# Kernel tuning notes

Measured on AMD Instinct MI355X. Metric: run time of the kernel, lower is better.

The kernel has to match this reference:

```python
import jax, jax.numpy as jnp
import numpy as np

N, E, DIN, H, EIN, EH, STEPS = 10000, 100000, 64, 64, 16, 128, 3


def setup_inputs() -> dict:
    key = jax.random.key(0)
    ks = jax.random.split(key, 8)
    n_feat = jax.random.normal(ks[0], (N, DIN), jnp.float32)
    e_feat = jax.random.normal(ks[1], (E, EIN), jnp.float32)
    src = jax.random.randint(ks[2], (E,), 0, N, jnp.int32)
    dst = jax.random.randint(ks[3], (E,), 0, N, jnp.int32)
    W0 = jax.random.normal(ks[4], (DIN, H), jnp.float32) / np.sqrt(DIN)
    b0 = jnp.zeros((H,), jnp.float32)
    We1 = jax.random.normal(ks[5], (EIN, EH), jnp.float32) / np.sqrt(EIN)
    be1 = jnp.zeros((EH,), jnp.float32)
    # small scale so per-edge HxH weight matrices keep activations stable
    We2 = jax.random.normal(ks[6], (EH, H * H), jnp.float32) * 0.02
    be2 = jnp.zeros((H * H,), jnp.float32)
    conv_bias = jnp.zeros((H,), jnp.float32)
    gamma = jnp.ones((H,), jnp.float32)
    beta = jnp.zeros((H,), jnp.float32)
    return {"n_feat": n_feat, "e_feat": e_feat, "src": src, "dst": dst,
            "W0": W0, "b0": b0, "We1": We1, "be1": be1, "We2": We2,
            "be2": be2, "conv_bias": conv_bias, "gamma": gamma, "beta": beta}


def reference(n_feat, e_feat, src, dst, W0, b0, We1, be1, We2, be2, conv_bias, gamma, beta):
    n = n_feat.shape[0]
    h = W0.shape[1]
    out = jax.nn.relu(n_feat @ W0 + b0)  # [N,H]
    # edge network (eval mode: dropout = identity); e_feat is fixed so the
    # per-edge weight matrices are identical each step -> compute once.
    w_edge = (jax.nn.relu(e_feat @ We1 + be1) @ We2 + be2).reshape(-1, h, h)  # [E,H,H]
    for _ in range(STEPS):
        msg = jnp.einsum('ei,eio->eo', out[src], w_edge)  # gather + per-edge matmul
        agg = jax.ops.segment_sum(msg, dst, num_segments=n)  # scatter-sum to dst
        out = jax.nn.relu(agg + conv_bias)
    # BatchNorm1d over nodes (training-mode batch statistics)
    mean = jnp.mean(out, axis=0)
    var = jnp.var(out, axis=0)
    return (out - mean) * jax.lax.rsqrt(var + 1e-5) * gamma + beta
```

## Files before the change

### kernel.cpp

```cpp
#include <hip/hip_runtime.h>
#include <stdint.h>

#define DIN   64
#define HDIM  64
#define EIN   16
#define EHID  128
#define HH    4096
#define TC    8256
#define STEPS 3

typedef short bf16x8 __attribute__((ext_vector_type(8)));
typedef float f32x4  __attribute__((ext_vector_type(4)));

__device__ __forceinline__ unsigned short f32_to_bf16(float f) {
    union { float f; uint32_t u; } v; v.f = f;
    uint32_t r = v.u + 0x7fffu + ((v.u >> 16) & 1u);
    return (unsigned short)(r >> 16);
}
__device__ __forceinline__ float bfu_to_f(unsigned short u) {
    union { uint32_t u; float f; } v; v.u = (uint32_t)u << 16; return v.f;
}

__global__ void k_pro(const float* __restrict__ nf, const float* __restrict__ W0,
                      const float* __restrict__ b0, float* __restrict__ outb,
                      unsigned short* __restrict__ outbf,
                      const float* __restrict__ ef, const float* __restrict__ We1,
                      const float* __restrict__ be1, unsigned short* __restrict__ h,
                      const float* __restrict__ We2, const float* __restrict__ be2,
                      unsigned short* __restrict__ BmatT,
                      const int* __restrict__ src, const int* __restrict__ dst,
                      int* __restrict__ cntS, int* __restrict__ cntD,
                      int n_nodes, int n_edges, int nbN, int nbE, int nbB) {
    __shared__ float smem[DIN * HDIM];
    int b = blockIdx.x, tid = threadIdx.x;
    if (b < nbN) {
        for (int i = tid; i < DIN * HDIM; i += 256) smem[i] = W0[i];
        __syncthreads();
        int node = b * 4 + (tid >> 6);
        int o = tid & 63;
        if (node >= n_nodes) return;
        float xr = nf[node * DIN + o];
        float acc = b0[o];
#pragma unroll 8
        for (int i = 0; i < DIN; ++i)
            acc += __shfl(xr, i, 64) * smem[i * HDIM + o];
        float v = fmaxf(acc, 0.f);
        outb[node * HDIM + o] = v;
        outbf[node * HDIM + o] = f32_to_bf16(v);
    } else if (b < nbN + nbE) {
        float* w1s = smem;
        float* xs  = smem + EIN * EHID;
        int e0 = (b - nbN) * 16;
#pragma unroll
        for (int i = tid; i < EIN * EHID; i += 256) w1s[i] = We1[i];
        xs[tid] = ef[(size_t)e0 * EIN + tid];
        __syncthreads();
        int g = tid >> 4, c0 = (tid & 15) * 8;
        int edge = e0 + g;
        if (edge >= n_edges) return;
        float acc[8];
#pragma unroll
        for (int j = 0; j < 8; ++j) acc[j] = be1[c0 + j];
#pragma unroll
        for (int i = 0; i < EIN; ++i) {
            float xi = xs[g * EIN + i];
#pragma unroll
            for (int j = 0; j < 8; ++j) acc[j] += xi * w1s[i * EHID + c0 + j];
        }
        uint32_t p0 = f32_to_bf16(fmaxf(acc[0], 0.f)) | ((uint32_t)f32_to_bf16(fmaxf(acc[1], 0.f)) << 16);
        uint32_t p1 = f32_to_bf16(fmaxf(acc[2], 0.f)) | ((uint32_t)f32_to_bf16(fmaxf(acc[3], 0.f)) << 16);
        uint32_t p2 = f32_to_bf16(fmaxf(acc[4], 0.f)) | ((uint32_t)f32_to_bf16(fmaxf(acc[5], 0.f)) << 16);
        uint32_t p3 = f32_to_bf16(fmaxf(acc[6], 0.f)) | ((uint32_t)f32_to_bf16(fmaxf(acc[7], 0.f)) << 16);
        uint4 pk = {p0, p1, p2, p3};
        *(uint4*)(h + (size_t)edge * EHID + c0) = pk;
    } else if (b < nbN + nbE + nbB) {
        int t = (b - nbN - nbE) * 256 + tid;
        if (t >= TC * 64) return;
        int c = t >> 6, i = t & 63;
        int g = c & 63;
        int m = (c & ~63) + 4 * (g & 15) + (g >> 4);
        float v;
        if (m < 8192) {
            int k = ((m >> 11) << 5) | (m & 31);
            int o = (m >> 5) & 63;
            v = We2[k * HH + i * 64 + o];
        } else {
            v = be2[i * 64 + (m - 8192)];
        }
        BmatT[t] = f32_to_bf16(v);
    } else {
        int e = (b - nbN - nbE - nbB) * 256 + tid;
        if (e >= n_edges) return;
        atomicAdd(&cntS[src[e]], 1);
        atomicAdd(&cntD[dst[e]], 1);
    }
}

__global__ void k_T(const unsigned short* __restrict__ outbf, const unsigned short* __restrict__ BmatT,
                    unsigned short* __restrict__ T, int n0, int n1) {
    int wave = threadIdx.x >> 6, lane = threadIdx.x & 63;
    int r = lane & 15, q = lane >> 4;
    int eb = n0 + blockIdx.y * 128;
    int cb = blockIdx.x * 256 + wave * 64;
    bf16x8 bfr[4][2];
#pragma unroll
    for (int nt = 0; nt < 4; ++nt) {
        int c = cb + nt * 16 + r;
        if (c >= TC) c = 0;
        size_t cofs = (size_t)c * 64;
        bfr[nt][0] = *(const bf16x8*)(BmatT + cofs + q * 8);
        bfr[nt][1] = *(const bf16x8*)(BmatT + cofs + 32 + q * 8);
    }
    bool cok = (cb < TC);
#pragma unroll
    for (int mt = 0; mt < 8; ++mt) {
        int e = eb + mt * 16 + r;
        if (e >= n1) e = n1 - 1;
        bf16x8 afr0 = *(const bf16x8*)(outbf + (size_t)e * 64 + q * 8);
        bf16x8 afr1 = *(const bf16x8*)(outbf + (size_t)e * 64 + 32 + q * 8);
        f32x4 acc[4] = {};
#pragma unroll
        for (int nt = 0; nt < 4; ++nt) {
            acc[nt] = __builtin_amdgcn_mfma_f32_16x16x32_bf16(afr0, bfr[nt][0], acc[nt], 0, 0, 0);
            acc[nt] = __builtin_amdgcn_mfma_f32_16x16x32_bf16(afr1, bfr[nt][1], acc[nt], 0, 0, 0);
        }
        if (!cok) continue;
#pragma unroll
        for (int rg = 0; rg < 4; ++rg) {
            int n = eb + mt * 16 + q * 4 + rg;
            if (n >= n1) continue;
            ushort4 pk;
            pk.x = f32_to_bf16(acc[0][rg]);
            pk.y = f32_to_bf16(acc[1][rg]);
            pk.z = f32_to_bf16(acc[2][rg]);
            pk.w = f32_to_bf16(acc[3][rg]);
            *(ushort4*)(T + (size_t)(n - n0) * TC + cb + 4 * r) = pk;
        }
    }
}

__global__ void k_msg(const unsigned short* __restrict__ h, const unsigned short* __restrict__ T,
                      const int* __restrict__ offS, const int* __restrict__ permS,
                      float* __restrict__ msg, int n0, int n1) {
    int wave = threadIdx.x >> 6, lane = threadIdx.x & 63;
    int n = n0 + blockIdx.x * 4 + wave;
    if (n >= n1) return;
    int beg = offS[n], end = offS[n + 1];
    if (beg == end) return;
    int r = lane & 15, q = lane >> 4;
    const unsigned short* Tb = T + (size_t)(n - n0) * TC;
    float bias[4];
#pragma unroll
    for (int nt = 0; nt < 4; ++nt)
        bias[nt] = bfu_to_f(Tb[8192 + nt * 16 + r]);
    for (int j0 = beg; j0 < end; j0 += 16) {
        int jc = j0 + r; if (jc >= end) jc = end - 1;
        int e = permS[jc];
        const unsigned short* he = h + (size_t)e * EHID;
        f32x4 acc[4] = {};
#pragma unroll
        for (int s = 0; s < 4; ++s) {
            bf16x8 afr = *(const bf16x8*)(he + s * 32 + q * 8);
#pragma unroll
            for (int nt = 0; nt < 4; ++nt) {
                bf16x8 bfr = *(const bf16x8*)(Tb + s * 2048 + (nt * 16 + r) * 32 + q * 8);
                acc[nt] = __builtin_amdgcn_mfma_f32_16x16x32_bf16(afr, bfr, acc[nt], 0, 0, 0);
            }
        }
#pragma unroll
        for (int rg = 0; rg < 4; ++rg) {
            int jr = j0 + q * 4 + rg;
            if (jr >= end) continue;
            int er = permS[jr];
#pragma unroll
            for (int nt = 0; nt < 4; ++nt)
                msg[(size_t)er * 64 + nt * 16 + r] = acc[nt][rg] + bias[nt];
        }
    }
}

__global__ void k_scan(const int* __restrict__ cntS, const int* __restrict__ cntD,
                       int* __restrict__ offS, int* __restrict__ offD,
                       int* __restrict__ curS, int* __restrict__ curD, int n, int total) {
    const int* cnt = blockIdx.x ? cntD : cntS;
    int* off = blockIdx.x ? offD : offS;
    int* cur = blockIdx.x ? curD : curS;
    __shared__ int part[256];
    int tid = threadIdx.x;
    int chunk = (n + 255) / 256;
    int c0 = tid * chunk, c1 = c0 + chunk; if (c1 > n) c1 = n; if (c0 > n) c0 = n;
    int s = 0;
    for (int i = c0; i < c1; ++i) s += cnt[i];
    part[tid] = s;
    __syncthreads();
    for (int st = 1; st < 256; st <<= 1) {
        int v = (tid >= st) ? part[tid - st] : 0;
        __syncthreads();
        part[tid] += v;
        __syncthreads();
    }
    int run = tid ? part[tid - 1] : 0;
    for (int i = c0; i < c1; ++i) { off[i] = run; cur[i] = run; run += cnt[i]; }
    if (tid == 0) off[n] = total;
}

__global__ void k_perm(const int* __restrict__ src, const int* __restrict__ dst,
                       int* __restrict__ curS, int* __restrict__ curD,
                       int* __restrict__ permS, int* __restrict__ permD, int n_edges) {
    int e = blockIdx.x * 256 + threadIdx.x;
    if (e >= n_edges) return;
    permS[atomicAdd(&curS[src[e]], 1)] = e;
    permD[atomicAdd(&curD[dst[e]], 1)] = e;
}

__global__ void k_agg(const float* __restrict__ msg, const int* __restrict__ offD,
                      const int* __restrict__ permD, const float* __restrict__ cbias,
                      float* __restrict__ outb, unsigned short* __restrict__ outbf, int n_nodes) {
    int wave = threadIdx.x >> 6, lane = threadIdx.x & 63;
    int d = blockIdx.x * 4 + wave;
    if (d >= n_nodes) return;
    float acc = 0.f;
    int end = offD[d + 1];
    for (int j = offD[d]; j < end; ++j)
        acc += msg[(size_t)permD[j] * 64 + lane];
    float v = fmaxf(acc + cbias[lane], 0.f);
    outb[(size_t)d * 64 + lane] = v;
    outbf[(size_t)d * 64 + lane] = f32_to_bf16(v);
}

__global__ void k_bn_stats(const float* __restrict__ out, float* __restrict__ stat, int n_nodes) {
    __shared__ float s1[256], s2[256];
    int tid = threadIdx.x;
    int f = tid & 63, g = tid >> 6;
    float sum = 0.f, ss = 0.f;
    for (int r = blockIdx.x * 4 + g; r < n_nodes; r += 256) {
        float v = out[r * HDIM + f];
        sum += v; ss += v * v;
    }
    s1[tid] = sum; s2[tid] = ss;
    __syncthreads();
    if (tid < 64) {
        float A = s1[tid] + s1[64 + tid] + s1[128 + tid] + s1[192 + tid];
        float B = s2[tid] + s2[64 + tid] + s2[128 + tid] + s2[192 + tid];
        atomicAdd(&stat[tid], A);
        atomicAdd(&stat[64 + tid], B);
    }
}

__global__ void k_bn_apply(const float* __restrict__ out, const float* __restrict__ stat,
                           const float* __restrict__ gamma, const float* __restrict__ beta,
                           float* __restrict__ y, int n, int n_nodes) {
    int t = blockIdx.x * 256 + threadIdx.x;
    if (t >= n) return;
    int f = t & 63;
    float mean = stat[f] / n_nodes;
    float var  = stat[64 + f] / n_nodes - mean * mean;
    float inv  = rsqrtf(var + 1e-5f);
    float scale = gamma[f] * inv;
    float shift = beta[f] - mean * scale;
    y[t] = out[t] * scale + shift;
}

extern "C" void kernel_launch(void* const* d_in, const int* in_sizes, int n_in,
                              void* d_out, int out_size, void* d_ws, size_t ws_size,
                              hipStream_t stream) {
    const float* nf    = (const float*)d_in[0];
    const float* ef    = (const float*)d_in[1];
    const int*   src   = (const int*)d_in[2];
    const int*   dst   = (const int*)d_in[3];
    const float* W0    = (const float*)d_in[4];
    const float* b0    = (const float*)d_in[5];
    const float* We1   = (const float*)d_in[6];
    const float* be1   = (const float*)d_in[7];
    const float* We2   = (const float*)d_in[8];
    const float* be2   = (const float*)d_in[9];
    const float* cbias = (const float*)d_in[10];
    const float* gamma = (const float*)d_in[11];
    const float* beta  = (const float*)d_in[12];
    (void)n_in; (void)out_size;

    int n_nodes = in_sizes[0] / DIN;
    int n_edges = in_sizes[2];

    char* ws = (char*)d_ws;
    size_t off = 0;
    auto carve = [&](size_t bytes) -> void* {
        void* p = ws + off;
        off = (off + bytes + 255) & ~(size_t)255;
        return p;
    };
    unsigned short* h     = (unsigned short*)carve((size_t)n_edges * EHID * 2);
    float*          msg   = (float*)carve((size_t)n_edges * 64 * 4);
    float*          outb  = (float*)carve((size_t)n_nodes * HDIM * 4);
    unsigned short* outbf = (unsigned short*)carve((size_t)n_nodes * HDIM * 2);
    unsigned short* BmatT = (unsigned short*)carve((size_t)TC * 64 * 2);
    int*            offS  = (int*)carve((size_t)(n_nodes + 1) * 4);
    int*            offD  = (int*)carve((size_t)(n_nodes + 1) * 4);
    int*            curS  = (int*)carve((size_t)n_nodes * 4);
    int*            curD  = (int*)carve((size_t)n_nodes * 4);
    int*            permS = (int*)carve((size_t)n_edges * 4);
    int*            permD = (int*)carve((size_t)n_edges * 4);
    float*          stat  = (float*)carve(128 * 4 + (size_t)2 * n_nodes * 4);
    int*            cntS  = (int*)(stat + 128);
    int*            cntD  = cntS + n_nodes;
    unsigned short* T     = (unsigned short*)(ws + off);
    size_t avail = ws_size > off ? ws_size - off : 0;
    long tcap = (long)(avail / ((size_t)TC * 2));
    if (tcap > n_nodes) tcap = n_nodes;
    if (tcap < 64) tcap = 64;
    long half = (((long)n_nodes + 1) / 2 + 63) & ~63L;
    long tchunk = tcap < half ? tcap : half;

    hipMemsetAsync(stat, 0, 128 * 4 + (size_t)2 * n_nodes * 4, stream);

    int nbN = (n_nodes + 3) / 4;
    int nbE = (n_edges + 15) / 16;
    int nbB = (TC * 64 + 255) / 256;
    int nbH = (n_edges + 255) / 256;
    k_pro<<<dim3(nbN + nbE + nbB + nbH), 256, 0, stream>>>(
        nf, W0, b0, outb, outbf, ef, We1, be1, h, We2, be2, BmatT,
        src, dst, cntS, cntD, n_nodes, n_edges, nbN, nbE, nbB);
    k_scan<<<dim3(2), 256, 0, stream>>>(cntS, cntD, offS, offD, curS, curD, n_nodes, n_edges);
    k_perm<<<dim3((n_edges + 255) / 256), 256, 0, stream>>>(src, dst, curS, curD, permS, permD, n_edges);

    for (int step = 0; step < STEPS; ++step) {
        for (long n0 = 0; n0 < n_nodes; n0 += tchunk) {
            long n1 = n0 + tchunk; if (n1 > n_nodes) n1 = n_nodes;
            long cnt = n1 - n0;
            k_T<<<dim3((TC + 255) / 256, (cnt + 127) / 128), 256, 0, stream>>>(
                outbf, BmatT, T, (int)n0, (int)n1);
            k_msg<<<dim3((cnt + 3) / 4), 256, 0, stream>>>(
                h, T, offS, permS, msg, (int)n0, (int)n1);
        }
        k_agg<<<dim3((n_nodes + 3) / 4), 256, 0, stream>>>(msg, offD, permD, cbias, outb, outbf, n_nodes);
    }

    k_bn_stats<<<dim3(64), 256, 0, stream>>>(outb, stat, n_nodes);
    k_bn_apply<<<dim3((n_nodes * HDIM + 255) / 256), 256, 0, stream>>>(
        outb, stat, gamma, beta, (float*)d_out, n_nodes * HDIM, n_nodes);
}
```

Before: 481.3 us.

## Compute edge hidden layer with MFMA and drop forced node-chunk halving

```diff
diff --git a/kernel.cpp b/kernel.cpp
--- a/kernel.cpp
+++ b/kernel.cpp
@@ -48,31 +48,48 @@
         outb[node * HDIM + o] = v;
         outbf[node * HDIM + o] = f32_to_bf16(v);
     } else if (b < nbN + nbE) {
-        float* w1s = smem;
-        float* xs  = smem + EIN * EHID;
-        int e0 = (b - nbN) * 16;
-#pragma unroll
-        for (int i = tid; i < EIN * EHID; i += 256) w1s[i] = We1[i];
-        xs[tid] = ef[(size_t)e0 * EIN + tid];
-        __syncthreads();
-        int g = tid >> 4, c0 = (tid & 15) * 8;
-        int edge = e0 + g;
-        if (edge >= n_edges) return;
-        float acc[8];
-#pragma unroll
-        for (int j = 0; j < 8; ++j) acc[j] = be1[c0 + j];
-#pragma unroll
-        for (int i = 0; i < EIN; ++i) {
-            float xi = xs[g * EIN + i];
-#pragma unroll
-            for (int j = 0; j < 8; ++j) acc[j] += xi * w1s[i * EHID + c0 + j];
-        }
-        uint32_t p0 = f32_to_bf16(fmaxf(acc[0], 0.f)) | ((uint32_t)f32_to_bf16(fmaxf(acc[1], 0.f)) << 16);
-        uint32_t p1 = f32_to_bf16(fmaxf(acc[2], 0.f)) | ((uint32_t)f32_to_bf16(fmaxf(acc[3], 0.f)) << 16);
-        uint32_t p2 = f32_to_bf16(fmaxf(acc[4], 0.f)) | ((uint32_t)f32_to_bf16(fmaxf(acc[5], 0.f)) << 16);
-        uint32_t p3 = f32_to_bf16(fmaxf(acc[6], 0.f)) | ((uint32_t)f32_to_bf16(fmaxf(acc[7], 0.f)) << 16);
-        uint4 pk = {p0, p1, p2, p3};
-        *(uint4*)(h + (size_t)edge * EHID + c0) = pk;
+        int wave = tid >> 6, lane = tid & 63;
+        int r = lane & 15, q = lane >> 4;
+        int e0 = (b - nbN) * 64 + wave * 16;
+        if (e0 >= n_edges) return;
+        bf16x8 afr = (bf16x8){};
+        bf16x8 bfr[8];
+#pragma unroll
+        for (int nt = 0; nt < 8; ++nt) bfr[nt] = (bf16x8){};
+        if (q < 2) {
+            int ea = e0 + r; if (ea >= n_edges) ea = n_edges - 1;
+            const float* xa = ef + (size_t)ea * EIN + q * 8;
+#pragma unroll
+            for (int j = 0; j < 8; ++j) afr[j] = (short)f32_to_bf16(xa[j]);
+#pragma unroll
+            for (int nt = 0; nt < 8; ++nt)
+#pragma unroll
+                for (int j = 0; j < 8; ++j)
+                    bfr[nt][j] = (short)f32_to_bf16(We1[(q * 8 + j) * EHID + nt * 16 + r]);
+        }
+        f32x4 acc[8];
+#pragma unroll
+        for (int nt = 0; nt < 8; ++nt)
+            acc[nt] = __builtin_amdgcn_mfma_f32_16x16x32_bf16(afr, bfr[nt], (f32x4){}, 0, 0, 0);
+        float bias[8];
+#pragma unroll
+        for (int nt = 0; nt < 8; ++nt) bias[nt] = be1[nt * 16 + r];
+#pragma unroll
+        for (int rg = 0; rg < 4; ++rg) {
+            int e = e0 + q * 4 + rg;
+            if (e >= n_edges) continue;
+            ushort4 pk0, pk1;
+            pk0.x = f32_to_bf16(fmaxf(acc[0][rg] + bias[0], 0.f));
+            pk0.y = f32_to_bf16(fmaxf(acc[1][rg] + bias[1], 0.f));
+            pk0.z = f32_to_bf16(fmaxf(acc[2][rg] + bias[2], 0.f));
+            pk0.w = f32_to_bf16(fmaxf(acc[3][rg] + bias[3], 0.f));
+            pk1.x = f32_to_bf16(fmaxf(acc[4][rg] + bias[4], 0.f));
+            pk1.y = f32_to_bf16(fmaxf(acc[5][rg] + bias[5], 0.f));
+            pk1.z = f32_to_bf16(fmaxf(acc[6][rg] + bias[6], 0.f));
+            pk1.w = f32_to_bf16(fmaxf(acc[7][rg] + bias[7], 0.f));
+            *(ushort4*)(h + (size_t)e * EHID + 4 * r) = pk0;
+            *(ushort4*)(h + (size_t)e * EHID + 64 + 4 * r) = pk1;
+        }
     } else if (b < nbN + nbE + nbB) {
         int t = (b - nbN - nbE) * 256 + tid;
         if (t >= TC * 64) return;
@@ -81,7 +98,8 @@
         int m = (c & ~63) + 4 * (g & 15) + (g >> 4);
         float v;
         if (m < 8192) {
-            int k = ((m >> 11) << 5) | (m & 31);
+            int p = ((m >> 11) << 5) | (m & 31);
+            int k = (p & 64) + ((p & 3) << 4) + ((p >> 2) & 15);
             int o = (m >> 5) & 63;
             v = We2[k * HH + i * 64 + o];
         } else {
@@ -308,13 +326,12 @@
     long tcap = (long)(avail / ((size_t)TC * 2));
     if (tcap > n_nodes) tcap = n_nodes;
     if (tcap < 64) tcap = 64;
-    long half = (((long)n_nodes + 1) / 2 + 63) & ~63L;
-    long tchunk = tcap < half ? tcap : half;
+    long tchunk = tcap;
 
     hipMemsetAsync(stat, 0, 128 * 4 + (size_t)2 * n_nodes * 4, stream);
 
     int nbN = (n_nodes + 3) / 4;
-    int nbE = (n_edges + 15) / 16;
+    int nbE = (n_edges + 63) / 64;
     int nbB = (TC * 64 + 255) / 256;
     int nbH = (n_edges + 255) / 256;
     k_pro<<<dim3(nbN + nbE + nbB + nbH), 256, 0, stream>>>(
```

After: 436.7 us. -9.3%, faster.
